# Performance work log

Hardware: AMD Instinct MI355X
Metric: run time of the kernel (lower is better)

The kernel has to match this reference:

```python
import jax, jax.numpy as jnp
import numpy as np

THETA = 0.5


def setup_inputs() -> dict:
    key = jax.random.key(0)
    k1, k2, k3 = jax.random.split(key, 3)
    B, S, D = 64, 4096, 256
    # strictly increasing times with small positive deltas
    dt = jax.random.uniform(k1, (B, S, 1), dtype=jnp.float32) * 0.01 + 1e-4
    t = jnp.cumsum(dt, axis=-2)
    x0 = jax.random.normal(k2, (B, 1, D), dtype=jnp.float32)
    z = jax.random.normal(k3, (B, S, D), dtype=jnp.float32)
    return {"t": t, "x0": x0, "z": z}


def reference(t, x0, z):
    # t: [B,S,1], x0: [B,1,D], z: [B,S,D]
    # OU recurrence: x_i = c_i * x_{i-1} + sqrt(1 - c_i^2) * z_i,  c_i = exp(-theta * dt_i)
    delta = jnp.diff(t, axis=-2, prepend=jnp.zeros_like(t[..., :1, :]))  # [B,S,1]
    c = jnp.exp(-THETA * delta)                                          # [B,S,1]
    b = jnp.sqrt(1.0 - c * c) * z                                        # [B,S,D]
    # fold initial state into step 0: b_0 += c_0 * x0
    b = b.at[..., 0, :].add(c[..., 0, :] * x0[..., 0, :])
    a = jnp.broadcast_to(c, b.shape)                                     # [B,S,D]

    def combine(e1, e2):
        a1, b1 = e1
        a2, b2 = e2
        return (a2 * a1, a2 * b1 + b2)

    _, x = jax.lax.associative_scan(combine, (a, b), axis=-2)
    return x  # [B,S,D]
```

## Files before the change

kernel.cpp:

```cpp
#include <hip/hip_runtime.h>


#define THETA 0.5f
constexpr int Bn = 64;
constexpr int Sn = 4096;
constexpr int Dn = 256;
constexpr int CHUNK = 64;
constexpr int NC = Sn / CHUNK;
constexpr int WPB = 4;
constexpr int NCB = NC / WPB;
constexpr int PF = 8;

typedef float f32x4 __attribute__((ext_vector_type(4)));

__global__ __launch_bounds__(256) void k_agg(
    const float* __restrict__ t,
    const float* __restrict__ x0,
    const float* __restrict__ z,
    float* __restrict__ agg)
{
    const int w    = threadIdx.x >> 6;
    const int lane = threadIdx.x & 63;
    const int b    = blockIdx.x / NCB;
    const int k    = (blockIdx.x % NCB) * WPB + w;
    const int s0   = k * CHUNK;

    __shared__ float2 css[WPB][CHUNK];
    {
        const int r = s0 + lane;
        const float tcur  = t[b * Sn + r];
        const float tprev = (r == 0) ? 0.0f : t[b * Sn + r - 1];
        const float c = __expf(-THETA * (tcur - tprev));
        css[w][lane] = make_float2(c, sqrtf(fmaxf(0.0f, 1.0f - c * c)));
    }
    __syncthreads();

    const int d0 = lane * 4;
    float a0 = 0.f, a1 = 0.f, a2 = 0.f, a3 = 0.f;
    if (k == 0) {
        const f32x4 xv = *(const f32x4*)(x0 + (size_t)b * Dn + d0);
        a0 = xv.x; a1 = xv.y; a2 = xv.z; a3 = xv.w;
    }

    const float* zp = z + ((size_t)b * Sn + s0) * Dn + d0;
    f32x4 buf[PF];
#pragma unroll
    for (int i = 0; i < PF; ++i)
        buf[i] = *(const f32x4*)(zp + (size_t)i * Dn);
#pragma unroll
    for (int r = 0; r < CHUNK; ++r) {
        const f32x4 zv = buf[r & (PF - 1)];
        if (r + PF < CHUNK)
            buf[r & (PF - 1)] = *(const f32x4*)(zp + (size_t)(r + PF) * Dn);
        const float2 cv = css[w][r];
        a0 = fmaf(cv.x, a0, cv.y * zv.x);
        a1 = fmaf(cv.x, a1, cv.y * zv.y);
        a2 = fmaf(cv.x, a2, cv.y * zv.z);
        a3 = fmaf(cv.x, a3, cv.y * zv.w);
    }

    f32x4 av; av.x = a0; av.y = a1; av.z = a2; av.w = a3;
    *(f32x4*)(agg + ((size_t)b * NC + k) * Dn + d0) = av;
}

__global__ __launch_bounds__(64) void k_scan(
    const float* __restrict__ t,
    float* __restrict__ agg)
{
    const int b    = blockIdx.x >> 2;
    const int tile = blockIdx.x & 3;
    const int lane = threadIdx.x;
    const int d    = tile * 64 + lane;

    __shared__ float As[NC];
    {
        const float tend = t[b * Sn + lane * CHUNK + CHUNK - 1];
        const float tpe  = (lane == 0) ? 0.0f : t[b * Sn + lane * CHUNK - 1];
        As[lane] = __expf(-THETA * (tend - tpe));
    }
    __syncthreads();

    float* ap = agg + (size_t)b * NC * Dn + d;
    float cin = 0.0f;
    float buf[PF];
#pragma unroll
    for (int i = 0; i < PF; ++i) buf[i] = ap[(size_t)i * Dn];
#pragma unroll
    for (int k = 0; k < NC; ++k) {
        const float bk = buf[k & (PF - 1)];
        if (k + PF < NC) buf[k & (PF - 1)] = ap[(size_t)(k + PF) * Dn];
        ap[(size_t)k * Dn] = cin;
        cin = fmaf(As[k], cin, bk);
    }
}

__global__ __launch_bounds__(256) void k_final(
    const float* __restrict__ t,
    const float* __restrict__ x0,
    const float* __restrict__ z,
    const float* __restrict__ carry,
    float* __restrict__ out)
{
    const int w    = threadIdx.x >> 6;
    const int lane = threadIdx.x & 63;
    const int b    = blockIdx.x / NCB;
    const int k    = (blockIdx.x % NCB) * WPB + w;
    const int s0   = k * CHUNK;

    __shared__ float2 css[WPB][CHUNK];
    {
        const int r = s0 + lane;
        const float tcur  = t[b * Sn + r];
        const float tprev = (r == 0) ? 0.0f : t[b * Sn + r - 1];
        const float c = __expf(-THETA * (tcur - tprev));
        css[w][lane] = make_float2(c, sqrtf(fmaxf(0.0f, 1.0f - c * c)));
    }
    __syncthreads();

    const int d0 = lane * 4;
    float a0, a1, a2, a3;
    if (k == 0) {
        const f32x4 xv = *(const f32x4*)(x0 + (size_t)b * Dn + d0);
        a0 = xv.x; a1 = xv.y; a2 = xv.z; a3 = xv.w;
    } else {
        const f32x4 cv = *(const f32x4*)(carry + ((size_t)b * NC + k) * Dn + d0);
        a0 = cv.x; a1 = cv.y; a2 = cv.z; a3 = cv.w;
    }

    const float* zp = z + ((size_t)b * Sn + s0) * Dn + d0;
    float* op = out + ((size_t)b * Sn + s0) * Dn + d0;

    f32x4 buf[PF];
#pragma unroll
    for (int i = 0; i < PF; ++i)
        buf[i] = __builtin_nontemporal_load((const f32x4*)(zp + (size_t)i * Dn));
#pragma unroll
    for (int r = 0; r < CHUNK; ++r) {
        const f32x4 zv = buf[r & (PF - 1)];
        if (r + PF < CHUNK)
            buf[r & (PF - 1)] =
                __builtin_nontemporal_load((const f32x4*)(zp + (size_t)(r + PF) * Dn));
        const float2 cv = css[w][r];
        a0 = fmaf(cv.x, a0, cv.y * zv.x);
        a1 = fmaf(cv.x, a1, cv.y * zv.y);
        a2 = fmaf(cv.x, a2, cv.y * zv.z);
        a3 = fmaf(cv.x, a3, cv.y * zv.w);
        f32x4 ov; ov.x = a0; ov.y = a1; ov.z = a2; ov.w = a3;
        __builtin_nontemporal_store(ov, (f32x4*)(op + (size_t)r * Dn));
    }
}

extern "C" void kernel_launch(void* const* d_in, const int* in_sizes, int n_in,
                              void* d_out, int out_size, void* d_ws, size_t ws_size,
                              hipStream_t stream) {
    const float* t  = (const float*)d_in[0];
    const float* x0 = (const float*)d_in[1];
    const float* z  = (const float*)d_in[2];
    float* out = (float*)d_out;

    float* agg = (float*)d_ws;

    k_agg  <<<Bn * NCB, 256, 0, stream>>>(t, x0, z, agg);
    k_scan <<<Bn * 4,    64, 0, stream>>>(t, agg);
    k_final<<<Bn * NCB, 256, 0, stream>>>(t, x0, z, agg, out);
}
```

Before: 482.4 us.

## Fold chunk-carry scan into final kernel and drop separate scan launch

Removes the k_scan kernel. Each block of k_final now computes its chunk's incoming carry by serially folding all preceding chunk aggregates with per-chunk decay factors held in shared memory. This removes one launch and the serial scan stage between the two main passes. In exchange, every chunk re-reads up to 63 aggregate rows, which adds redundant cache traffic and latency, growing with chunk index. The nontemporal load hints are also shuffled: k_agg's initial z prefetch becomes nontemporal, and k_final's in-loop z loads become ordinary loads.

New measurement: 487.3 us. No clear change (+1.0%).

```diff
diff --git a/kernel.cpp b/kernel.cpp
--- a/kernel.cpp
+++ b/kernel.cpp
@@ -46,7 +46,7 @@
     f32x4 buf[PF];
 #pragma unroll
     for (int i = 0; i < PF; ++i)
-        buf[i] = *(const f32x4*)(zp + (size_t)i * Dn);
+        buf[i] = __builtin_nontemporal_load((const f32x4*)(zp + (size_t)i * Dn));
 #pragma unroll
     for (int r = 0; r < CHUNK; ++r) {
         const f32x4 zv = buf[r & (PF - 1)];
@@ -63,42 +63,11 @@
     *(f32x4*)(agg + ((size_t)b * NC + k) * Dn + d0) = av;
 }
 
-__global__ __launch_bounds__(64) void k_scan(
-    const float* __restrict__ t,
-    float* __restrict__ agg)
-{
-    const int b    = blockIdx.x >> 2;
-    const int tile = blockIdx.x & 3;
-    const int lane = threadIdx.x;
-    const int d    = tile * 64 + lane;
-
-    __shared__ float As[NC];
-    {
-        const float tend = t[b * Sn + lane * CHUNK + CHUNK - 1];
-        const float tpe  = (lane == 0) ? 0.0f : t[b * Sn + lane * CHUNK - 1];
-        As[lane] = __expf(-THETA * (tend - tpe));
-    }
-    __syncthreads();
-
-    float* ap = agg + (size_t)b * NC * Dn + d;
-    float cin = 0.0f;
-    float buf[PF];
-#pragma unroll
-    for (int i = 0; i < PF; ++i) buf[i] = ap[(size_t)i * Dn];
-#pragma unroll
-    for (int k = 0; k < NC; ++k) {
-        const float bk = buf[k & (PF - 1)];
-        if (k + PF < NC) buf[k & (PF - 1)] = ap[(size_t)(k + PF) * Dn];
-        ap[(size_t)k * Dn] = cin;
-        cin = fmaf(As[k], cin, bk);
-    }
-}
-
 __global__ __launch_bounds__(256) void k_final(
     const float* __restrict__ t,
     const float* __restrict__ x0,
     const float* __restrict__ z,
-    const float* __restrict__ carry,
+    const float* __restrict__ agg,
     float* __restrict__ out)
 {
     const int w    = threadIdx.x >> 6;
@@ -108,12 +77,19 @@
     const int s0   = k * CHUNK;
 
     __shared__ float2 css[WPB][CHUNK];
+    __shared__ float  As[NC];
     {
         const int r = s0 + lane;
         const float tcur  = t[b * Sn + r];
         const float tprev = (r == 0) ? 0.0f : t[b * Sn + r - 1];
         const float c = __expf(-THETA * (tcur - tprev));
         css[w][lane] = make_float2(c, sqrtf(fmaxf(0.0f, 1.0f - c * c)));
+    }
+    if (threadIdx.x < NC) {
+        const int j = threadIdx.x;
+        const float tend = t[b * Sn + j * CHUNK + CHUNK - 1];
+        const float tpe  = (j == 0) ? 0.0f : t[b * Sn + j * CHUNK - 1];
+        As[j] = __expf(-THETA * (tend - tpe));
     }
     __syncthreads();
 
@@ -123,8 +99,26 @@
         const f32x4 xv = *(const f32x4*)(x0 + (size_t)b * Dn + d0);
         a0 = xv.x; a1 = xv.y; a2 = xv.z; a3 = xv.w;
     } else {
-        const f32x4 cv = *(const f32x4*)(carry + ((size_t)b * NC + k) * Dn + d0);
-        a0 = cv.x; a1 = cv.y; a2 = cv.z; a3 = cv.w;
+        float c0 = 0.f, c1 = 0.f, c2 = 0.f, c3 = 0.f;
+        const float* gp = agg + (size_t)b * NC * Dn + d0;
+        int j = 0;
+        for (; j + 4 <= k; j += 4) {
+            const f32x4 g0 = *(const f32x4*)(gp + (size_t)(j + 0) * Dn);
+            const f32x4 g1 = *(const f32x4*)(gp + (size_t)(j + 1) * Dn);
+            const f32x4 g2 = *(const f32x4*)(gp + (size_t)(j + 2) * Dn);
+            const f32x4 g3 = *(const f32x4*)(gp + (size_t)(j + 3) * Dn);
+            float A;
+            A = As[j + 0]; c0 = fmaf(A, c0, g0.x); c1 = fmaf(A, c1, g0.y); c2 = fmaf(A, c2, g0.z); c3 = fmaf(A, c3, g0.w);
+            A = As[j + 1]; c0 = fmaf(A, c0, g1.x); c1 = fmaf(A, c1, g1.y); c2 = fmaf(A, c2, g1.z); c3 = fmaf(A, c3, g1.w);
+            A = As[j + 2]; c0 = fmaf(A, c0, g2.x); c1 = fmaf(A, c1, g2.y); c2 = fmaf(A, c2, g2.z); c3 = fmaf(A, c3, g2.w);
+            A = As[j + 3]; c0 = fmaf(A, c0, g3.x); c1 = fmaf(A, c1, g3.y); c2 = fmaf(A, c2, g3.z); c3 = fmaf(A, c3, g3.w);
+        }
+        for (; j < k; ++j) {
+            const f32x4 g = *(const f32x4*)(gp + (size_t)j * Dn);
+            const float A = As[j];
+            c0 = fmaf(A, c0, g.x); c1 = fmaf(A, c1, g.y); c2 = fmaf(A, c2, g.z); c3 = fmaf(A, c3, g.w);
+        }
+        a0 = c0; a1 = c1; a2 = c2; a3 = c3;
     }
 
     const float* zp = z + ((size_t)b * Sn + s0) * Dn + d0;
@@ -138,8 +132,7 @@
     for (int r = 0; r < CHUNK; ++r) {
         const f32x4 zv = buf[r & (PF - 1)];
         if (r + PF < CHUNK)
-            buf[r & (PF - 1)] =
-                __builtin_nontemporal_load((const f32x4*)(zp + (size_t)(r + PF) * Dn));
+            buf[r & (PF - 1)] = *(const f32x4*)(zp + (size_t)(r + PF) * Dn);
         const float2 cv = css[w][r];
         a0 = fmaf(cv.x, a0, cv.y * zv.x);
         a1 = fmaf(cv.x, a1, cv.y * zv.y);
@@ -161,6 +154,5 @@
     float* agg = (float*)d_ws;
 
     k_agg  <<<Bn * NCB, 256, 0, stream>>>(t, x0, z, agg);
-    k_scan <<<Bn * 4,    64, 0, stream>>>(t, agg);
     k_final<<<Bn * NCB, 256, 0, stream>>>(t, x0, z, agg, out);
 }
```
